# Kernel optimization log

Measured on AMD Instinct MI355X. Metric: run time of the kernel, lower is better.

## Reference

```python
import jax, jax.numpy as jnp
import numpy as np

K_NEAREST = 5
EPS = 1e-6


def setup_inputs() -> dict:
    key = jax.random.key(0)
    k1, k2, k3 = jax.random.split(key, 3)
    N_Q, N_DB, D_OUT, D_AUX = 4096, 65536, 32, 32
    return {
        "embedding_features": jax.random.normal(k1, (N_Q, D_OUT), dtype=jnp.float32),
        "db_embedding": jax.random.normal(k2, (N_DB, D_OUT), dtype=jnp.float32),
        "auxiliary_features": jax.random.normal(k3, (N_DB, D_AUX), dtype=jnp.float32),
    }


def reference(embedding_features, db_embedding, auxiliary_features):
    d_out = embedding_features.shape[-1]
    q = embedding_features.reshape(-1, d_out)          # [Nq, D]
    db = db_embedding.reshape(-1, d_out)               # [Ndb, D]

    # Euclidean cdist via the expanded quadratic form (same math as torch.cdist p=2).
    q_sq = jnp.sum(q * q, axis=1, keepdims=True)       # [Nq, 1]
    db_sq = jnp.sum(db * db, axis=1)[None, :]          # [1, Ndb]
    dist_sq = q_sq + db_sq - 2.0 * (q @ db.T)          # [Nq, Ndb]
    distances = jnp.sqrt(jnp.maximum(dist_sq, 0.0))

    # k smallest distances == k largest of negated distances.
    neg_top, nearest_indices = jax.lax.top_k(-distances, K_NEAREST)  # [Nq, k]
    nearest_distances = -neg_top                                      # [Nq, k]

    aux = auxiliary_features.reshape(-1, auxiliary_features.shape[-1])
    nearest_aux = aux[nearest_indices]                 # [Nq, k, Daux]

    weights = 1.0 / (nearest_distances + EPS)
    weights = weights / jnp.sum(weights, axis=1, keepdims=True)

    return jnp.sum(nearest_aux * weights[..., None], axis=1)  # [Nq, Daux]
```

## Files before the change

kernel.cpp:

```cpp
#include <hip/hip_runtime.h>
#include <math.h>

#define N_Q   4096
#define N_DB  65536
#define DIM   32
#define KNN   5
#define NC    64
#define CH    (N_DB / NC)
#define NSUB  32
#define NCAND (NC * 6)
#define BIAS  256.0f

typedef _Float16 half8  __attribute__((ext_vector_type(8)));
typedef __fp16   fp16x2 __attribute__((ext_vector_type(2)));
typedef float floatx16  __attribute__((ext_vector_type(16)));

union H8  { half8 h; uint4 u4; unsigned u[4]; };
union F16 { floatx16 v; float4 q4[4]; unsigned w[16]; };
union HU  { fp16x2 h2; unsigned u; };

__device__ __forceinline__ unsigned cvt2(float a, float b) {
    HU t; t.h2 = __builtin_amdgcn_cvt_pkrtz(a, b);
    return t.u;
}

__global__ __launch_bounds__(256) void k_prep(const float* __restrict__ DB,
                                              uint4* __restrict__ DBh,
                                              float* __restrict__ hdb) {
    int p = blockIdx.x * 256 + threadIdx.x;
    const float4* src = (const float4*)(DB + (size_t)p * DIM);
    float4 f[8]; float s = 0.f;
#pragma unroll
    for (int j = 0; j < 8; ++j) {
        f[j] = src[j];
        s += f[j].x * f[j].x + f[j].y * f[j].y + f[j].z * f[j].z + f[j].w * f[j].w;
    }
    hdb[p] = BIAS - 0.5f * s;
    int t = p >> 5, r = p & 31;
#pragma unroll
    for (int gi = 0; gi < 4; ++gi) {
        uint4 g;
        g.x = cvt2(f[2 * gi].x, f[2 * gi].y);
        g.y = cvt2(f[2 * gi].z, f[2 * gi].w);
        g.z = cvt2(f[2 * gi + 1].x, f[2 * gi + 1].y);
        g.w = cvt2(f[2 * gi + 1].z, f[2 * gi + 1].w);
        DBh[(size_t)t * 128 + gi * 32 + r] = g;
    }
}

__global__ __launch_bounds__(256, 6) void k_scan(const float* __restrict__ Q,
                                                 const uint4* __restrict__ DBh,
                                                 const float* __restrict__ hdb,
                                                 unsigned* __restrict__ cand) {
    const int tid = threadIdx.x, lane = tid & 63, w = tid >> 6;
    const int h = lane >> 5, qcol = lane & 31;
    const int chunk = blockIdx.x & (NC - 1);
    const int qb    = blockIdx.x >> 6;
    const int q     = qb * 128 + w * 32 + qcol;
    const int pbase = chunk * CH;

    const float* qp = Q + (size_t)q * DIM;
    float4 qa = *(const float4*)(qp + h * 8);
    float4 qb4 = *(const float4*)(qp + h * 8 + 4);
    float4 qc = *(const float4*)(qp + 16 + h * 8);
    float4 qd = *(const float4*)(qp + 16 + h * 8 + 4);
    H8 b1, b2;
    b1.u[0] = cvt2(qa.x, qa.y);   b1.u[1] = cvt2(qa.z, qa.w);
    b1.u[2] = cvt2(qb4.x, qb4.y); b1.u[3] = cvt2(qb4.z, qb4.w);
    b2.u[0] = cvt2(qc.x, qc.y);   b2.u[1] = cvt2(qc.z, qc.w);
    b2.u[2] = cvt2(qd.x, qd.y);   b2.u[3] = cvt2(qd.z, qd.w);

    unsigned maskv;
    asm("v_mov_b32 %0, 0xFFFFFC00" : "=v"(maskv));

    const uint4* abase = DBh + (size_t)(pbase >> 5) * 128 + h * 32 + (lane & 31);
    const float* hb0   = hdb + pbase + 4 * h;

    float tk[6];
#pragma unroll
    for (int r = 0; r < 6; ++r) tk[r] = 0.f;

    constexpr int ROWC[16] = {0,1,2,3, 8,9,10,11, 16,17,18,19, 24,25,26,27};

    auto compute = [&](const H8& A1, const H8& A2, const int s) {
        const float* hbp = hb0 + s * 32;
        F16 c0;
        c0.q4[0] = *(const float4*)(hbp + 0);
        c0.q4[1] = *(const float4*)(hbp + 8);
        c0.q4[2] = *(const float4*)(hbp + 16);
        c0.q4[3] = *(const float4*)(hbp + 24);
        floatx16 acc = __builtin_amdgcn_mfma_f32_32x32x16_f16(A1.h, b1.h, c0.v, 0, 0, 0);
        acc = __builtin_amdgcn_mfma_f32_32x32x16_f16(A2.h, b2.h, acc, 0, 0, 0);
        F16 pk; pk.v = acc;
        const int meta = s << 5;
        float p[16];
#pragma unroll
        for (int r = 0; r < 16; ++r)
            p[r] = __uint_as_float((pk.w[r] & maskv) | (unsigned)(meta | ROWC[r]));
        float hi[8], lo[8];
#pragma unroll
        for (int i = 0; i < 8; ++i) { hi[i] = fmaxf(p[2*i], p[2*i+1]); lo[i] = fminf(p[2*i], p[2*i+1]); }
        float H4[4], L4[4];
#pragma unroll
        for (int i = 0; i < 4; ++i) {
            H4[i] = fmaxf(hi[2*i], hi[2*i+1]);
            L4[i] = fmaxf(fmaxf(lo[2*i], lo[2*i+1]), fminf(hi[2*i], hi[2*i+1]));
        }
        float H2[2], L2[2];
#pragma unroll
        for (int i = 0; i < 2; ++i) {
            H2[i] = fmaxf(H4[2*i], H4[2*i+1]);
            L2[i] = fmaxf(fmaxf(L4[2*i], L4[2*i+1]), fminf(H4[2*i], H4[2*i+1]));
        }
        float c1 = fmaxf(H2[0], H2[1]);
        float c2 = fmaxf(fmaxf(L2[0], L2[1]), fminf(H2[0], H2[1]));
        {
            float m01 = fminf(tk[0], c1), m02 = fminf(tk[1], c1);
            float m03 = fminf(tk[2], c1), m04 = fminf(tk[3], c1);
            float m05 = fminf(tk[4], c1);
            float m12 = fminf(tk[0], c2), m13 = fminf(tk[1], c2);
            float m14 = fminf(tk[2], c2), m15 = fminf(tk[3], c2);
            tk[0] = fmaxf(tk[0], c1);
            tk[1] = fmaxf(fmaxf(tk[1], m01), c2);
            tk[2] = fmaxf(fmaxf(tk[2], m02), m12);
            tk[3] = fmaxf(fmaxf(tk[3], m03), m13);
            tk[4] = fmaxf(fmaxf(tk[4], m04), m14);
            tk[5] = fmaxf(fmaxf(tk[5], m05), m15);
        }
    };

    H8 a1A, a2A, a1B, a2B;
    a1A.u4 = abase[0];
    a2A.u4 = abase[64];
    for (int s = 0; s < NSUB; s += 2) {
        a1B.u4 = abase[(size_t)(s + 1) * 128];
        a2B.u4 = abase[(size_t)(s + 1) * 128 + 64];
        compute(a1A, a2A, s);
        if (s + 2 < NSUB) {
            a1A.u4 = abase[(size_t)(s + 2) * 128];
            a2A.u4 = abase[(size_t)(s + 2) * 128 + 64];
        }
        compute(a1B, a2B, s + 1);
    }

#pragma unroll
    for (int r = 0; r < 6; ++r)
        tk[r] = __uint_as_float(__float_as_uint(tk[r]) | (unsigned)(h << 2));

    float other[6];
#pragma unroll
    for (int i = 0; i < 6; ++i) other[i] = __shfl_xor(tk[i], 32, 64);
#pragma unroll
    for (int i = 0; i < 6; ++i) {
        float val = other[i];
#pragma unroll
        for (int j = 0; j < 6; ++j) { float mx = fmaxf(tk[j], val); val = fminf(tk[j], val); tk[j] = mx; }
    }
    if (h == 0) {
        unsigned* dst = cand + ((size_t)q * NC + chunk) * 6;
#pragma unroll
        for (int r = 0; r < 6; ++r) dst[r] = __float_as_uint(tk[r]);
    }
}

__global__ __launch_bounds__(256) void k_merge(const float* __restrict__ Q,
                                               const float* __restrict__ DB,
                                               const float* __restrict__ AUX,
                                               const unsigned* __restrict__ cand,
                                               float* __restrict__ out) {
    const int tid = threadIdx.x, lane = tid & 63, w = tid >> 6;
    const int q = blockIdx.x * 4 + w;

    const unsigned* cq = cand + (size_t)q * NCAND + (size_t)lane * 6;
    float cur[6];
#pragma unroll
    for (int r = 0; r < 6; ++r) cur[r] = __uint_as_float(cq[r]);

    float wv[12]; int wl[12];
#pragma unroll
    for (int r = 0; r < 12; ++r) {
        float bv = cur[0]; int bl = lane;
#pragma unroll
        for (int off = 32; off >= 1; off >>= 1) {
            float ov = __shfl_xor(bv, off, 64);
            int   ol = __shfl_xor(bl, off, 64);
            if (ov > bv || (ov == bv && ol < bl)) { bv = ov; bl = ol; }
        }
        wv[r] = bv; wl[r] = bl;
        if (bl == lane) {
#pragma unroll
            for (int s = 0; s < 5; ++s) cur[s] = cur[s + 1];
            cur[5] = -1.f;
        }
    }

    float dist = 1e30f; int dbi = 0x7fffffff;
    if (lane < 12) {
        unsigned u = __float_as_uint(wv[lane]) & 1023u;
        dbi = wl[lane] * CH + (int)u;
        const float4* dp = (const float4*)(DB + (size_t)dbi * DIM);
        const float4* qp = (const float4*)(Q + (size_t)q * DIM);
        float dot = 0.f, qs = 0.f, ds = 0.f;
#pragma unroll
        for (int j = 0; j < DIM / 4; ++j) {
            float4 a = qp[j], d = dp[j];
            dot += a.x * d.x + a.y * d.y + a.z * d.z + a.w * d.w;
            qs  += a.x * a.x + a.y * a.y + a.z * a.z + a.w * a.w;
            ds  += d.x * d.x + d.y * d.y + d.z * d.z + d.w * d.w;
        }
        dist = sqrtf(fmaxf(qs + ds - 2.f * dot, 0.f));
    }
    float wd[KNN]; int wi[KNN];
#pragma unroll
    for (int r = 0; r < KNN; ++r) {
        float bd = dist; int bi = dbi;
#pragma unroll
        for (int off = 32; off >= 1; off >>= 1) {
            float od = __shfl_xor(bd, off, 64);
            int   oi = __shfl_xor(bi, off, 64);
            if (od < bd || (od == bd && oi < bi)) { bd = od; bi = oi; }
        }
        wd[r] = bd; wi[r] = bi;
        if (dist == bd && dbi == bi) dist = 1e30f;
    }
    float ww[KNN], W = 0.f;
#pragma unroll
    for (int r = 0; r < KNN; ++r) { ww[r] = 1.f / (wd[r] + 1e-6f); W += ww[r]; }
    if (lane < DIM) {
        float o = 0.f;
#pragma unroll
        for (int r = 0; r < KNN; ++r) o += ww[r] * AUX[(size_t)wi[r] * DIM + lane];
        out[(size_t)q * DIM + lane] = o / W;
    }
}

extern "C" void kernel_launch(void* const* d_in, const int* in_sizes, int n_in,
                              void* d_out, int out_size, void* d_ws, size_t ws_size,
                              hipStream_t stream) {
    const float* Q   = (const float*)d_in[0];
    const float* DB  = (const float*)d_in[1];
    const float* AUX = (const float*)d_in[2];
    float* out = (float*)d_out;

    char* ws = (char*)d_ws;
    uint4*    DBh = (uint4*)ws;                         ws += (size_t)(N_DB / 32) * 128 * 16;
    float*    hdb = (float*)ws;                         ws += (size_t)N_DB * 4;
    unsigned* cand = (unsigned*)ws;

    k_prep<<<N_DB / 256, 256, 0, stream>>>(DB, DBh, hdb);
    k_scan<<<(N_Q / 128) * NC, 256, 0, stream>>>(Q, DBh, hdb, cand);
    k_merge<<<N_Q / 4, 256, 0, stream>>>(Q, DB, AUX, cand, out);
}
```

Before: 143.0 us.

## Fold database norm bias into an extra MFMA and deepen the load pipeline

The per-point bias (BIAS - 0.5*||db||^2) is now stored as an fp16 hi/lo pair and added through a third MFMA against a ones vector, instead of being loaded as four float4 accumulator inputs per subtile. The scan loop prefetches four subtiles ahead instead of two, and the occupancy hint drops from 6 to 5 blocks. This cuts global/L1 load traffic and load latency in the scan, at the cost of 50% more MFMA work per subtile and higher register pressure. The prefetch also reads up to two subtiles past each chunk's end, though those values are never used.

```diff
diff --git a/kernel.cpp b/kernel.cpp
--- a/kernel.cpp
+++ b/kernel.cpp
@@ -26,7 +26,7 @@
 
 __global__ __launch_bounds__(256) void k_prep(const float* __restrict__ DB,
                                               uint4* __restrict__ DBh,
-                                              float* __restrict__ hdb) {
+                                              unsigned* __restrict__ DBn) {
     int p = blockIdx.x * 256 + threadIdx.x;
     const float4* src = (const float4*)(DB + (size_t)p * DIM);
     float4 f[8]; float s = 0.f;
@@ -35,7 +35,10 @@
         f[j] = src[j];
         s += f[j].x * f[j].x + f[j].y * f[j].y + f[j].z * f[j].z + f[j].w * f[j].w;
     }
-    hdb[p] = BIAS - 0.5f * s;
+    float v  = BIAS - 0.5f * s;
+    float hi = (float)(__fp16)v;
+    float lo = v - hi;
+    DBn[p] = cvt2(hi, lo);
     int t = p >> 5, r = p & 31;
 #pragma unroll
     for (int gi = 0; gi < 4; ++gi) {
@@ -48,15 +51,15 @@
     }
 }
 
-__global__ __launch_bounds__(256, 6) void k_scan(const float* __restrict__ Q,
+__global__ __launch_bounds__(256, 5) void k_scan(const float* __restrict__ Q,
                                                  const uint4* __restrict__ DBh,
-                                                 const float* __restrict__ hdb,
+                                                 const unsigned* __restrict__ DBn,
                                                  unsigned* __restrict__ cand) {
     const int tid = threadIdx.x, lane = tid & 63, w = tid >> 6;
-    const int h = lane >> 5, qcol = lane & 31;
+    const int h = lane >> 5, row = lane & 31;
     const int chunk = blockIdx.x & (NC - 1);
     const int qb    = blockIdx.x >> 6;
-    const int q     = qb * 128 + w * 32 + qcol;
+    const int q     = qb * 128 + w * 32 + row;
     const int pbase = chunk * CH;
 
     const float* qp = Q + (size_t)q * DIM;
@@ -64,17 +67,24 @@
     float4 qb4 = *(const float4*)(qp + h * 8 + 4);
     float4 qc = *(const float4*)(qp + 16 + h * 8);
     float4 qd = *(const float4*)(qp + 16 + h * 8 + 4);
-    H8 b1, b2;
+    H8 b1, b2, b3;
     b1.u[0] = cvt2(qa.x, qa.y);   b1.u[1] = cvt2(qa.z, qa.w);
     b1.u[2] = cvt2(qb4.x, qb4.y); b1.u[3] = cvt2(qb4.z, qb4.w);
     b2.u[0] = cvt2(qc.x, qc.y);   b2.u[1] = cvt2(qc.z, qc.w);
     b2.u[2] = cvt2(qd.x, qd.y);   b2.u[3] = cvt2(qd.z, qd.w);
+    b3.u[0] = (h == 0) ? cvt2(1.f, 1.f) : 0u;
+    b3.u[1] = 0u; b3.u[2] = 0u; b3.u[3] = 0u;
+    const unsigned hmask = (h == 0) ? 0xFFFFFFFFu : 0u;
 
     unsigned maskv;
     asm("v_mov_b32 %0, 0xFFFFFC00" : "=v"(maskv));
 
-    const uint4* abase = DBh + (size_t)(pbase >> 5) * 128 + h * 32 + (lane & 31);
-    const float* hb0   = hdb + pbase + 4 * h;
+    const uint4*    abase = DBh + (size_t)(pbase >> 5) * 128 + h * 32 + row;
+    const unsigned* nbase = DBn + pbase + row;
+
+    floatx16 zc;
+#pragma unroll
+    for (int r = 0; r < 16; ++r) zc[r] = 0.f;
 
     float tk[6];
 #pragma unroll
@@ -82,14 +92,12 @@
 
     constexpr int ROWC[16] = {0,1,2,3, 8,9,10,11, 16,17,18,19, 24,25,26,27};
 
-    auto compute = [&](const H8& A1, const H8& A2, const int s) {
-        const float* hbp = hb0 + s * 32;
-        F16 c0;
-        c0.q4[0] = *(const float4*)(hbp + 0);
-        c0.q4[1] = *(const float4*)(hbp + 8);
-        c0.q4[2] = *(const float4*)(hbp + 16);
-        c0.q4[3] = *(const float4*)(hbp + 24);
-        floatx16 acc = __builtin_amdgcn_mfma_f32_32x32x16_f16(A1.h, b1.h, c0.v, 0, 0, 0);
+    auto compute = [&](const H8& A1, const H8& A2, unsigned A3u, const int s) {
+        H8 a3;
+        a3.u[0] = A3u & hmask;
+        a3.u[1] = 0u; a3.u[2] = 0u; a3.u[3] = 0u;
+        floatx16 acc = __builtin_amdgcn_mfma_f32_32x32x16_f16(a3.h, b3.h, zc, 0, 0, 0);
+        acc = __builtin_amdgcn_mfma_f32_32x32x16_f16(A1.h, b1.h, acc, 0, 0, 0);
         acc = __builtin_amdgcn_mfma_f32_32x32x16_f16(A2.h, b2.h, acc, 0, 0, 0);
         F16 pk; pk.v = acc;
         const int meta = s << 5;
@@ -97,14 +105,14 @@
 #pragma unroll
         for (int r = 0; r < 16; ++r)
             p[r] = __uint_as_float((pk.w[r] & maskv) | (unsigned)(meta | ROWC[r]));
-        float hi[8], lo[8];
-#pragma unroll
-        for (int i = 0; i < 8; ++i) { hi[i] = fmaxf(p[2*i], p[2*i+1]); lo[i] = fminf(p[2*i], p[2*i+1]); }
+        float hi8[8], lo8[8];
+#pragma unroll
+        for (int i = 0; i < 8; ++i) { hi8[i] = fmaxf(p[2*i], p[2*i+1]); lo8[i] = fminf(p[2*i], p[2*i+1]); }
         float H4[4], L4[4];
 #pragma unroll
         for (int i = 0; i < 4; ++i) {
-            H4[i] = fmaxf(hi[2*i], hi[2*i+1]);
-            L4[i] = fmaxf(fmaxf(lo[2*i], lo[2*i+1]), fminf(hi[2*i], hi[2*i+1]));
+            H4[i] = fmaxf(hi8[2*i], hi8[2*i+1]);
+            L4[i] = fmaxf(fmaxf(lo8[2*i], lo8[2*i+1]), fminf(hi8[2*i], hi8[2*i+1]));
         }
         float H2[2], L2[2];
 #pragma unroll
@@ -129,18 +137,22 @@
         }
     };
 
-    H8 a1A, a2A, a1B, a2B;
-    a1A.u4 = abase[0];
-    a2A.u4 = abase[64];
-    for (int s = 0; s < NSUB; s += 2) {
-        a1B.u4 = abase[(size_t)(s + 1) * 128];
-        a2B.u4 = abase[(size_t)(s + 1) * 128 + 64];
-        compute(a1A, a2A, s);
-        if (s + 2 < NSUB) {
-            a1A.u4 = abase[(size_t)(s + 2) * 128];
-            a2A.u4 = abase[(size_t)(s + 2) * 128 + 64];
-        }
-        compute(a1B, a2B, s + 1);
+    auto LD = [&](H8& x1, H8& x2, unsigned& x3, const int s) {
+        const uint4* ap = abase + (size_t)s * 128;
+        x1.u4 = ap[0];
+        x2.u4 = ap[64];
+        x3 = nbase[s * 32];
+    };
+
+    H8 sA1, sA2, sB1, sB2, sC1, sC2, sD1, sD2;
+    unsigned nA, nB, nC, nD;
+    LD(sA1, sA2, nA, 0);
+    LD(sB1, sB2, nB, 1);
+    for (int s = 0; s < NSUB; s += 4) {
+        LD(sC1, sC2, nC, s + 2);  compute(sA1, sA2, nA, s);
+        LD(sD1, sD2, nD, s + 3);  compute(sB1, sB2, nB, s + 1);
+        LD(sA1, sA2, nA, s + 4);  compute(sC1, sC2, nC, s + 2);
+        LD(sB1, sB2, nB, s + 5);  compute(sD1, sD2, nD, s + 3);
     }
 
 #pragma unroll
@@ -244,10 +256,10 @@
 
     char* ws = (char*)d_ws;
     uint4*    DBh = (uint4*)ws;                         ws += (size_t)(N_DB / 32) * 128 * 16;
-    float*    hdb = (float*)ws;                         ws += (size_t)N_DB * 4;
+    unsigned* DBn = (unsigned*)ws;                      ws += (size_t)N_DB * 4;
     unsigned* cand = (unsigned*)ws;
 
-    k_prep<<<N_DB / 256, 256, 0, stream>>>(DB, DBh, hdb);
-    k_scan<<<(N_Q / 128) * NC, 256, 0, stream>>>(Q, DBh, hdb, cand);
+    k_prep<<<N_DB / 256, 256, 0, stream>>>(DB, DBh, DBn);
+    k_scan<<<(N_Q / 128) * NC, 256, 0, stream>>>(Q, DBh, DBn, cand);
     k_merge<<<N_Q / 4, 256, 0, stream>>>(Q, DB, AUX, cand, out);
 }
```

After: 139.8 us. 2.3% less time.
